# Optimization experiments

Hardware: AMD Instinct MI355X
Metric: run time of the kernel (lower is better)

Reference implementation:

```python
import jax, jax.numpy as jnp
import numpy as np

K = 3  # TAGConv default number of hops
N, E = 50000, 800000
F_X, F_POS, HID, OUT = 6, 2, 64, 10


def _tagconv(x, W, b, src, dst, norm, n):
    # TAGConv: out = sum_{k=0}^{K} (A_norm^k x) @ W[k] + b
    out = x @ W[0]
    h = x
    for k in range(1, K + 1):
        # one propagate step: gather from src, weight, scatter-sum to dst
        h = jax.ops.segment_sum(norm[:, None] * h[src], dst, num_segments=n)
        out = out + h @ W[k]
    return out + b


def setup_inputs() -> dict:
    key = jax.random.key(0)
    ks = jax.random.split(key, 12)
    x = jax.random.normal(ks[0], (N, F_X), dtype=jnp.float32)
    pos = jax.random.normal(ks[1], (N, F_POS), dtype=jnp.float32)
    edge_index = jax.random.randint(ks[2], (2, E), 0, N, dtype=jnp.int64)
    edge_attr = jax.random.uniform(ks[3], (E,), dtype=jnp.float32)
    s = 0.1
    W1 = jax.random.normal(ks[4], (K + 1, F_X + F_POS, HID), dtype=jnp.float32) * s
    b1 = jnp.zeros((HID,), dtype=jnp.float32)
    W2 = jax.random.normal(ks[5], (K + 1, HID, HID), dtype=jnp.float32) * s
    b2 = jnp.zeros((HID,), dtype=jnp.float32)
    W3 = jax.random.normal(ks[6], (K + 1, HID, OUT), dtype=jnp.float32) * s
    b3 = jnp.zeros((OUT,), dtype=jnp.float32)
    return {"x": x, "pos": pos, "edge_attr": edge_attr,
            "W1": W1, "b1": b1, "W2": W2, "b2": b2, "W3": W3, "b3": b3,
            "edge_index": edge_index}


def reference(x, pos, edge_attr, W1, b1, W2, b2, W3, b3, edge_index):
    n = x.shape[0]
    src, dst = edge_index[0], edge_index[1]
    # gcn_norm (no self loops, as in TAGConv): deg over destination (col)
    deg = jax.ops.segment_sum(edge_attr, dst, num_segments=n)
    dinv = jnp.where(deg > 0, jax.lax.rsqrt(deg), jnp.zeros_like(deg))
    norm = dinv[src] * edge_attr * dinv[dst]
    h = jnp.concatenate([x, pos], axis=1)
    h = jax.nn.relu(_tagconv(h, W1, b1, src, dst, norm, n))
    # F.dropout with training=False is identity (eval reference)
    h = jax.nn.relu(_tagconv(h, W2, b2, src, dst, norm, n))
    h = _tagconv(h, W3, b3, src, dst, norm, n)
    return jax.nn.log_softmax(h, axis=1)
```

## Files before the change

kernel.cpp:

```cpp
#include <hip/hip_runtime.h>
#include <math.h>


#define NN 50000
#define EE 800000
#define HID 64
#define NOUT 10
#define CH 512

#define NB 391
#define CAP 2400
#define K1_EPB 4096

__device__ __forceinline__ unsigned bf16rnd(float x) {
    unsigned u = __float_as_uint(x);
    return (u + 0x7FFFu + ((u >> 16) & 1u)) >> 16;
}
__device__ __forceinline__ unsigned packbf2(float a, float b) {
    return bf16rnd(a) | (bf16rnd(b) << 16);
}
__device__ __forceinline__ float bflo(unsigned u) { return __uint_as_float(u << 16); }
__device__ __forceinline__ float bfhi(unsigned u) { return __uint_as_float(u & 0xFFFF0000u); }

__global__ __launch_bounds__(512) void bucket_scatter_kernel(
        const int* __restrict__ src, const int* __restrict__ dst,
        const float* __restrict__ ea, int* __restrict__ cursor,
        int2* __restrict__ regions, int e) {
    __shared__ int hist[NB];
    __shared__ int base[NB];
    int tid = threadIdx.x;
    int e0 = blockIdx.x * K1_EPB;
    int e1 = e0 + K1_EPB; if (e1 > e) e1 = e;
    for (int i = tid; i < NB; i += 512) hist[i] = 0;
    __syncthreads();
    for (int i = e0 + tid; i < e1; i += 512)
        atomicAdd(&hist[dst[i] >> 7], 1);
    __syncthreads();
    for (int b = tid; b < NB; b += 512) {
        int c = hist[b];
        base[b] = (c > 0) ? atomicAdd(&cursor[b], c) : 0;
        hist[b] = 0;
    }
    __syncthreads();
    for (int i = e0 + tid; i < e1; i += 512) {
        int d = dst[i];
        int b = d >> 7;
        int r = atomicAdd(&hist[b], 1);
        int pos = base[b] + r;
        if (pos < CAP)
            regions[(size_t)b * CAP + pos] =
                make_int2(((d & 127) << 16) | src[i], __float_as_int(ea[i]));
    }
}

__global__ __launch_bounds__(512) void bucket_build_kernel(
        const int* __restrict__ cursor, int2* __restrict__ regions,
        float* __restrict__ dinv, int* __restrict__ row_start, int n) {
    __shared__ int2 rec[CAP];
    __shared__ int hist[128];
    __shared__ float easum[128];
    __shared__ float dl[128];
    __shared__ int off[129];
    __shared__ int lcur[128];
    int b = blockIdx.x;
    int tid = threadIdx.x;
    int cnt = cursor[b]; if (cnt > CAP) cnt = CAP;
    size_t rb = (size_t)b * CAP;
    if (tid < 128) { hist[tid] = 0; easum[tid] = 0.f; lcur[tid] = 0; }
    __syncthreads();
    for (int i = tid; i < cnt; i += 512) {
        int2 r = regions[rb + i];
        rec[i] = r;
        int f = r.x >> 16;
        atomicAdd(&hist[f], 1);
        atomicAdd(&easum[f], __int_as_float(r.y));
    }
    __syncthreads();
    if (tid < 128) {
        int lane = tid & 63;
        int v = hist[tid];
        for (int o2 = 1; o2 < 64; o2 <<= 1) {
            int y = __shfl_up(v, o2, 64);
            if (lane >= o2) v += y;
        }
        off[tid + 1] = v;
        float s2 = easum[tid];
        dl[tid] = (s2 > 0.f) ? rsqrtf(s2) : 0.f;
    }
    __syncthreads();
    if (tid == 255) off[0] = 0;
    if (tid >= 64 && tid < 128) off[tid + 1] += off[64];
    __syncthreads();
    if (tid < 128) {
        int node = b * 128 + tid;
        if (node <= n) row_start[node] = b * CAP + off[tid];
        if (node < n)  dinv[node] = dl[tid];
    }
    __syncthreads();
    for (int i = tid; i < cnt; i += 512) {
        int2 r = rec[i];
        int f = r.x >> 16;
        int s = r.x & 0xFFFF;
        int p = atomicAdd(&lcur[f], 1);
        float w0 = __int_as_float(r.y) * dl[f];
        regions[rb + off[f] + p] = make_int2(s, __float_as_int(w0));
    }
}

__global__ __launch_bounds__(256) void srcscale_kernel(
        const int* __restrict__ cursor, const float* __restrict__ dinv,
        int2* __restrict__ regions) {
    int i = blockIdx.x * blockDim.x + threadIdx.x;
    int b = i / CAP;
    if (b >= NB) return;
    int off = i - b * CAP;
    int cnt = cursor[b]; if (cnt > CAP) cnt = CAP;
    if (off >= cnt) return;
    int2 r = regions[i];
    r.y = __float_as_int(__int_as_float(r.y) * dinv[r.x]);
    regions[i] = r;
}

__global__ __launch_bounds__(256) void pack1_kernel(const float* __restrict__ x,
                                                    const float* __restrict__ pos,
                                                    unsigned short* __restrict__ B1, int n) {
    int i = blockIdx.x * blockDim.x + threadIdx.x;
    if (i >= n) return;
    float2 a = *reinterpret_cast<const float2*>(x + (size_t)i * 6);
    float2 b = *reinterpret_cast<const float2*>(x + (size_t)i * 6 + 2);
    float2 c = *reinterpret_cast<const float2*>(x + (size_t)i * 6 + 4);
    float2 p = *reinterpret_cast<const float2*>(pos + (size_t)i * 2);
    uint4 o;
    o.x = packbf2(a.x, a.y);
    o.y = packbf2(b.x, b.y);
    o.z = packbf2(c.x, c.y);
    o.w = packbf2(p.x, p.y);
    *reinterpret_cast<uint4*>(B1 + (size_t)i * 32) = o;
}

__global__ __launch_bounds__(256) void prop8b_kernel(const int* __restrict__ row_start,
                                                     const int* __restrict__ cursor,
                                                     const int2* __restrict__ edges,
                                                     const unsigned short* __restrict__ Gin,
                                                     unsigned short* __restrict__ Gout, int n) {
    constexpr int TEAM = 8, NPB = 32;
    __shared__ int2 se[CH];
    int tid = threadIdx.x;
    int nb = blockIdx.x * NPB;
    int node = nb + tid / TEAM;
    int es = tid % TEAM;
    int nbEnd = (nb + NPB < n) ? (nb + NPB) : n;
    int bkt = nb >> 7;
    int cc = cursor[bkt]; if (cc > CAP) cc = CAP;
    int ce = bkt * CAP + cc;
    int blkBeg = row_start[nb];
    int blkEnd = row_start[nbEnd]; if (blkEnd > ce) blkEnd = ce;
    int beg = 0, end = 0;
    if (node < n) {
        beg = row_start[node];
        end = row_start[node + 1]; if (end > ce) end = ce;
    }
    float a0 = 0.f, a1 = 0.f, a2 = 0.f, a3 = 0.f, a4 = 0.f, a5 = 0.f, a6 = 0.f, a7 = 0.f;
    for (int base = blkBeg; base < blkEnd; base += CH) {
        int m = blkEnd - base; if (m > CH) m = CH;
        __syncthreads();
        for (int i = tid; i < m; i += 256) se[i] = edges[base + i];
        __syncthreads();
        int lo = (beg > base) ? (beg - base) : 0;
        int hi = ((end < base + m) ? end : (base + m)) - base;
        for (int i = lo + es; i < hi; i += TEAM) {
            int2 e = se[i];
            float w = __int_as_float(e.y);
            const uint4 v = *reinterpret_cast<const uint4*>(Gin + (size_t)e.x * 32);
            a0 += w * bflo(v.x); a1 += w * bfhi(v.x);
            a2 += w * bflo(v.y); a3 += w * bfhi(v.y);
            a4 += w * bflo(v.z); a5 += w * bfhi(v.z);
            a6 += w * bflo(v.w); a7 += w * bfhi(v.w);
        }
    }
    #pragma unroll
    for (int msk = 1; msk < TEAM; msk <<= 1) {
        a0 += __shfl_xor(a0, msk); a1 += __shfl_xor(a1, msk);
        a2 += __shfl_xor(a2, msk); a3 += __shfl_xor(a3, msk);
        a4 += __shfl_xor(a4, msk); a5 += __shfl_xor(a5, msk);
        a6 += __shfl_xor(a6, msk); a7 += __shfl_xor(a7, msk);
    }
    if (node < n && es == 0) {
        uint4 o;
        o.x = packbf2(a0, a1);
        o.y = packbf2(a2, a3);
        o.z = packbf2(a4, a5);
        o.w = packbf2(a6, a7);
        *reinterpret_cast<uint4*>(Gout + (size_t)node * 32) = o;
    }
}

template <int TPN, int ES, bool ACC>
__global__ __launch_bounds__(256) void prop_kernel(const int* __restrict__ row_start,
                                                   const int* __restrict__ cursor,
                                                   const int2* __restrict__ edges,
                                                   const float* __restrict__ hin, int in_stride,
                                                   float* __restrict__ hout, int out_stride, int n) {
    constexpr int TEAM = TPN * ES;
    constexpr int NPB = 256 / TEAM;
    __shared__ int2 se[CH];
    int tid = threadIdx.x;
    int nb = blockIdx.x * NPB;
    int node = nb + tid / TEAM;
    int t = tid % TEAM;
    int es = t / TPN;
    int lane = t % TPN;
    int nbEnd = (nb + NPB < n) ? (nb + NPB) : n;
    int bkt = nb >> 7;
    int cc = cursor[bkt]; if (cc > CAP) cc = CAP;
    int ce = bkt * CAP + cc;
    int blkBeg = row_start[nb];
    int blkEnd = row_start[nbEnd]; if (blkEnd > ce) blkEnd = ce;
    int beg = 0, end = 0;
    if (node < n) {
        beg = row_start[node];
        end = row_start[node + 1]; if (end > ce) end = ce;
    }
    float ax = 0.f, ay = 0.f, az = 0.f, aw = 0.f;
    for (int base = blkBeg; base < blkEnd; base += CH) {
        int m = blkEnd - base; if (m > CH) m = CH;
        __syncthreads();
        for (int i = tid; i < m; i += 256) se[i] = edges[base + i];
        __syncthreads();
        int lo = (beg > base) ? (beg - base) : 0;
        int hi = ((end < base + m) ? end : (base + m)) - base;
        for (int i = lo + es; i < hi; i += ES) {
            int2 e = se[i];
            float w = __int_as_float(e.y);
            const float4 v = *reinterpret_cast<const float4*>(hin + (size_t)e.x * in_stride + lane * 4);
            ax += w * v.x; ay += w * v.y; az += w * v.z; aw += w * v.w;
        }
    }
    #pragma unroll
    for (int msk = TPN; msk < TEAM; msk <<= 1) {
        ax += __shfl_xor(ax, msk);
        ay += __shfl_xor(ay, msk);
        az += __shfl_xor(az, msk);
        aw += __shfl_xor(aw, msk);
    }
    if (node < n && es == 0) {
        float4* po = reinterpret_cast<float4*>(hout + (size_t)node * out_stride + lane * 4);
        float4 r = make_float4(ax, ay, az, aw);
        if (ACC) { float4 o = *po; r.x += o.x; r.y += o.y; r.z += o.z; r.w += o.w; }
        *po = r;
    }
}

__global__ __launch_bounds__(256) void prop64b_kernel(const int* __restrict__ row_start,
                                                      const int* __restrict__ cursor,
                                                      const int2* __restrict__ edges,
                                                      const unsigned short* __restrict__ Gin,
                                                      unsigned short* __restrict__ Gout, int n) {
    constexpr int TPN = 8, ES = 4, TEAM = 32, NPB = 8;
    __shared__ int2 se[CH];
    int tid = threadIdx.x;
    int nb = blockIdx.x * NPB;
    int node = nb + tid / TEAM;
    int t = tid % TEAM;
    int es = t / TPN;
    int lane = t % TPN;
    int nbEnd = (nb + NPB < n) ? (nb + NPB) : n;
    int bkt = nb >> 7;
    int cc = cursor[bkt]; if (cc > CAP) cc = CAP;
    int ce = bkt * CAP + cc;
    int blkBeg = row_start[nb];
    int blkEnd = row_start[nbEnd]; if (blkEnd > ce) blkEnd = ce;
    int beg = 0, end = 0;
    if (node < n) {
        beg = row_start[node];
        end = row_start[node + 1]; if (end > ce) end = ce;
    }
    float a0 = 0.f, a1 = 0.f, a2 = 0.f, a3 = 0.f, a4 = 0.f, a5 = 0.f, a6 = 0.f, a7 = 0.f;
    for (int base = blkBeg; base < blkEnd; base += CH) {
        int m = blkEnd - base; if (m > CH) m = CH;
        __syncthreads();
        for (int i = tid; i < m; i += 256) se[i] = edges[base + i];
        __syncthreads();
        int lo = (beg > base) ? (beg - base) : 0;
        int hi = ((end < base + m) ? end : (base + m)) - base;
        for (int i = lo + es; i < hi; i += ES) {
            int2 e = se[i];
            float w = __int_as_float(e.y);
            const uint4 v = *reinterpret_cast<const uint4*>(Gin + (size_t)e.x * 256 + lane * 8);
            a0 += w * bflo(v.x); a1 += w * bfhi(v.x);
            a2 += w * bflo(v.y); a3 += w * bfhi(v.y);
            a4 += w * bflo(v.z); a5 += w * bfhi(v.z);
            a6 += w * bflo(v.w); a7 += w * bfhi(v.w);
        }
    }
    #pragma unroll
    for (int msk = TPN; msk < TEAM; msk <<= 1) {
        a0 += __shfl_xor(a0, msk); a1 += __shfl_xor(a1, msk);
        a2 += __shfl_xor(a2, msk); a3 += __shfl_xor(a3, msk);
        a4 += __shfl_xor(a4, msk); a5 += __shfl_xor(a5, msk);
        a6 += __shfl_xor(a6, msk); a7 += __shfl_xor(a7, msk);
    }
    if (node < n && es == 0) {
        uint4 o;
        o.x = packbf2(a0, a1);
        o.y = packbf2(a2, a3);
        o.z = packbf2(a4, a5);
        o.w = packbf2(a6, a7);
        *reinterpret_cast<uint4*>(Gout + (size_t)node * 256 + lane * 8) = o;
    }
}

__global__ __launch_bounds__(256) void prop_final_kernel(const int* __restrict__ row_start,
                                                         const int* __restrict__ cursor,
                                                         const int2* __restrict__ edges,
                                                         const float* __restrict__ hin,
                                                         const float* __restrict__ g0,
                                                         const float* __restrict__ b3,
                                                         float* __restrict__ out, int n) {
    constexpr int TPN = 4, ES = 2, TEAM = 8, NPB = 32;
    __shared__ int2 se[CH];
    int tid = threadIdx.x;
    int nb = blockIdx.x * NPB;
    int node = nb + tid / TEAM;
    int t = tid % TEAM;
    int es = t / TPN;
    int lane = t % TPN;
    int nbEnd = (nb + NPB < n) ? (nb + NPB) : n;
    int bkt = nb >> 7;
    int cc = cursor[bkt]; if (cc > CAP) cc = CAP;
    int ce = bkt * CAP + cc;
    int blkBeg = row_start[nb];
    int blkEnd = row_start[nbEnd]; if (blkEnd > ce) blkEnd = ce;
    int beg = 0, end = 0;
    if (node < n) {
        beg = row_start[node];
        end = row_start[node + 1]; if (end > ce) end = ce;
    }
    float ax = 0.f, ay = 0.f, az = 0.f, aw = 0.f;
    for (int base = blkBeg; base < blkEnd; base += CH) {
        int m = blkEnd - base; if (m > CH) m = CH;
        __syncthreads();
        for (int i = tid; i < m; i += 256) se[i] = edges[base + i];
        __syncthreads();
        int lo = (beg > base) ? (beg - base) : 0;
        int hi = ((end < base + m) ? end : (base + m)) - base;
        for (int i = lo + es; i < hi; i += ES) {
            int2 e = se[i];
            float w = __int_as_float(e.y);
            const float4 v = *reinterpret_cast<const float4*>(hin + (size_t)e.x * 64 + lane * 4);
            ax += w * v.x; ay += w * v.y; az += w * v.z; aw += w * v.w;
        }
    }
    ax += __shfl_xor(ax, TPN);
    ay += __shfl_xor(ay, TPN);
    az += __shfl_xor(az, TPN);
    aw += __shfl_xor(aw, TPN);
    if (node < n && es == 0) {
        const float4 g = *reinterpret_cast<const float4*>(g0 + (size_t)node * 64 + lane * 4);
        float vv[4] = {ax + g.x, ay + g.y, az + g.z, aw + g.w};
        int c0 = lane * 4;
        float mloc = -1e30f;
        #pragma unroll
        for (int c = 0; c < 4; ++c) {
            int col = c0 + c;
            if (col < NOUT) { vv[c] += b3[col]; mloc = fmaxf(mloc, vv[c]); }
        }
        float mo = fmaxf(mloc, __shfl_xor(mloc, 1));
        mo = fmaxf(mo, __shfl_xor(mo, 2));
        float sl = 0.f;
        #pragma unroll
        for (int c = 0; c < 4; ++c) {
            int col = c0 + c;
            if (col < NOUT) sl += __expf(vv[c] - mo);
        }
        sl += __shfl_xor(sl, 1);
        sl += __shfl_xor(sl, 2);
        float ls = __logf(sl);
        #pragma unroll
        for (int c = 0; c < 4; ++c) {
            int col = c0 + c;
            if (col < NOUT) out[(size_t)node * NOUT + col] = vv[c] - mo - ls;
        }
    }
}

template <int FIN, int KC, int EPI, int WMODE, int INBF16, int OUTBF16>
__global__ __launch_bounds__(256) void mm2_kernel(const void* __restrict__ hraw, int hstride,
                                                  const float* __restrict__ W,
                                                  const float* __restrict__ bias,
                                                  void* __restrict__ outraw, int ostride, int n) {
    constexpr int HP = 68;
    __shared__ float HsT[KC * HP];
    __shared__ float Ws[KC * 64];
    int tid = threadIdx.x;
    int ndq = tid >> 4;
    int f4  = tid & 15;
    int nd  = tid & 63;
    int wv  = tid >> 6;
    int nodeBase = blockIdx.x * 64;

    float4 acc0 = make_float4(0.f, 0.f, 0.f, 0.f);
    float4 acc1 = make_float4(0.f, 0.f, 0.f, 0.f);
    float4 acc2 = make_float4(0.f, 0.f, 0.f, 0.f);
    float4 acc3 = make_float4(0.f, 0.f, 0.f, 0.f);

    for (int kc = 0; kc < FIN; kc += KC) {
        if (WMODE == 0) {
            for (int i = tid * 4; i < KC * 64; i += 1024)
                *reinterpret_cast<float4*>(&Ws[i]) =
                    *reinterpret_cast<const float4*>(&W[(size_t)kc * 64 + i]);
        } else {
            for (int i = tid; i < KC * 64; i += 256) {
                int r = i >> 6, c = i & 63;
                int k = c >> 4, j = c & 15;
                Ws[i] = (j < NOUT) ? W[((size_t)k * FIN + kc + r) * NOUT + j] : 0.f;
            }
        }
        int node = nodeBase + nd;
        if constexpr (INBF16) {
            const unsigned short* hb = (const unsigned short*)hraw;
            constexpr int KPT = KC / 4;
            int k0 = wv * KPT;
            #pragma unroll
            for (int q = 0; q < KPT / 8; ++q) {
                uint4 v = make_uint4(0, 0, 0, 0);
                if (node < n)
                    v = *reinterpret_cast<const uint4*>(hb + (size_t)node * hstride + kc + k0 + q * 8);
                int kk = k0 + q * 8;
                HsT[(kk + 0) * HP + nd] = bflo(v.x); HsT[(kk + 1) * HP + nd] = bfhi(v.x);
                HsT[(kk + 2) * HP + nd] = bflo(v.y); HsT[(kk + 3) * HP + nd] = bfhi(v.y);
                HsT[(kk + 4) * HP + nd] = bflo(v.z); HsT[(kk + 5) * HP + nd] = bfhi(v.z);
                HsT[(kk + 6) * HP + nd] = bflo(v.w); HsT[(kk + 7) * HP + nd] = bfhi(v.w);
            }
        } else {
            const float* hf = (const float*)hraw;
            #pragma unroll
            for (int r = 0; r < KC / 16; ++r) {
                int k0 = wv * 4 + r * 16;
                float4 hv = make_float4(0.f, 0.f, 0.f, 0.f);
                if (node < n)
                    hv = *reinterpret_cast<const float4*>(&hf[(size_t)node * hstride + kc + k0]);
                HsT[(k0 + 0) * HP + nd] = hv.x;
                HsT[(k0 + 1) * HP + nd] = hv.y;
                HsT[(k0 + 2) * HP + nd] = hv.z;
                HsT[(k0 + 3) * HP + nd] = hv.w;
            }
        }
        __syncthreads();
        #pragma unroll 8
        for (int k = 0; k < KC; ++k) {
            const float4 hq = *reinterpret_cast<const float4*>(&HsT[k * HP + ndq * 4]);
            const float4 wq = *reinterpret_cast<const float4*>(&Ws[k * 64 + f4 * 4]);
            acc0.x += hq.x * wq.x; acc0.y += hq.x * wq.y; acc0.z += hq.x * wq.z; acc0.w += hq.x * wq.w;
            acc1.x += hq.y * wq.x; acc1.y += hq.y * wq.y; acc1.z += hq.y * wq.z; acc1.w += hq.y * wq.w;
            acc2.x += hq.z * wq.x; acc2.y += hq.z * wq.y; acc2.z += hq.z * wq.z; acc2.w += hq.z * wq.w;
            acc3.x += hq.w * wq.x; acc3.y += hq.w * wq.y; acc3.z += hq.w * wq.z; acc3.w += hq.w * wq.w;
        }
        __syncthreads();
    }

    float4 bv = make_float4(0.f, 0.f, 0.f, 0.f);
    if (EPI == 1) bv = *reinterpret_cast<const float4*>(&bias[f4 * 4]);
    float4 accs[4] = {acc0, acc1, acc2, acc3};
    #pragma unroll
    for (int i = 0; i < 4; ++i) {
        int node = nodeBase + ndq * 4 + i;
        if (node < n) {
            float4 a = accs[i];
            if (EPI == 1) {
                a.x = fmaxf(a.x + bv.x, 0.f); a.y = fmaxf(a.y + bv.y, 0.f);
                a.z = fmaxf(a.z + bv.z, 0.f); a.w = fmaxf(a.w + bv.w, 0.f);
            }
            if constexpr (OUTBF16) {
                unsigned short* ob = (unsigned short*)outraw;
                uint2 o;
                o.x = packbf2(a.x, a.y);
                o.y = packbf2(a.z, a.w);
                *reinterpret_cast<uint2*>(ob + (size_t)node * ostride + f4 * 4) = o;
            } else {
                float* of = (float*)outraw;
                *reinterpret_cast<float4*>(of + (size_t)node * ostride + f4 * 4) = a;
            }
        }
    }
}

__global__ __launch_bounds__(256) void mm23_kernel(const unsigned short* __restrict__ G,
                                                   const float* __restrict__ W2,
                                                   const float* __restrict__ b2,
                                                   const float* __restrict__ W3,
                                                   float* __restrict__ T, int n) {
    constexpr int HP = 68;
    __shared__ float HsT[64 * HP];
    __shared__ float Ws[64 * 64];
    int tid = threadIdx.x;
    int ndq = tid >> 4;
    int f4  = tid & 15;
    int nd  = tid & 63;
    int wv  = tid >> 6;
    int nodeBase = blockIdx.x * 64;

    float4 acc0 = make_float4(0.f, 0.f, 0.f, 0.f);
    float4 acc1 = make_float4(0.f, 0.f, 0.f, 0.f);
    float4 acc2 = make_float4(0.f, 0.f, 0.f, 0.f);
    float4 acc3 = make_float4(0.f, 0.f, 0.f, 0.f);

    for (int kc = 0; kc < 256; kc += 64) {
        for (int i = tid * 4; i < 64 * 64; i += 1024)
            *reinterpret_cast<float4*>(&Ws[i]) =
                *reinterpret_cast<const float4*>(&W2[(size_t)kc * 64 + i]);
        int node = nodeBase + nd;
        int k0 = wv * 16;
        uint4 q0 = make_uint4(0, 0, 0, 0), q1 = make_uint4(0, 0, 0, 0);
        if (node < n) {
            const unsigned short* row = G + (size_t)node * 256 + kc + k0;
            q0 = *reinterpret_cast<const uint4*>(row);
            q1 = *reinterpret_cast<const uint4*>(row + 8);
        }
        HsT[(k0 + 0) * HP + nd] = bflo(q0.x);  HsT[(k0 + 1) * HP + nd] = bfhi(q0.x);
        HsT[(k0 + 2) * HP + nd] = bflo(q0.y);  HsT[(k0 + 3) * HP + nd] = bfhi(q0.y);
        HsT[(k0 + 4) * HP + nd] = bflo(q0.z);  HsT[(k0 + 5) * HP + nd] = bfhi(q0.z);
        HsT[(k0 + 6) * HP + nd] = bflo(q0.w);  HsT[(k0 + 7) * HP + nd] = bfhi(q0.w);
        HsT[(k0 + 8) * HP + nd] = bflo(q1.x);  HsT[(k0 + 9) * HP + nd] = bfhi(q1.x);
        HsT[(k0 + 10) * HP + nd] = bflo(q1.y); HsT[(k0 + 11) * HP + nd] = bfhi(q1.y);
        HsT[(k0 + 12) * HP + nd] = bflo(q1.z); HsT[(k0 + 13) * HP + nd] = bfhi(q1.z);
        HsT[(k0 + 14) * HP + nd] = bflo(q1.w); HsT[(k0 + 15) * HP + nd] = bfhi(q1.w);
        __syncthreads();
        #pragma unroll 8
        for (int k = 0; k < 64; ++k) {
            const float4 hq = *reinterpret_cast<const float4*>(&HsT[k * HP + ndq * 4]);
            const float4 wq = *reinterpret_cast<const float4*>(&Ws[k * 64 + f4 * 4]);
            acc0.x += hq.x * wq.x; acc0.y += hq.x * wq.y; acc0.z += hq.x * wq.z; acc0.w += hq.x * wq.w;
            acc1.x += hq.y * wq.x; acc1.y += hq.y * wq.y; acc1.z += hq.y * wq.z; acc1.w += hq.y * wq.w;
            acc2.x += hq.z * wq.x; acc2.y += hq.z * wq.y; acc2.z += hq.z * wq.z; acc2.w += hq.z * wq.w;
            acc3.x += hq.w * wq.x; acc3.y += hq.w * wq.y; acc3.z += hq.w * wq.z; acc3.w += hq.w * wq.w;
        }
        __syncthreads();
    }

    {
        const float4 bv = *reinterpret_cast<const float4*>(&b2[f4 * 4]);
        float4 accs[4] = {acc0, acc1, acc2, acc3};
        #pragma unroll
        for (int i = 0; i < 4; ++i) {
            float4 a = accs[i];
            a.x = fmaxf(a.x + bv.x, 0.f); a.y = fmaxf(a.y + bv.y, 0.f);
            a.z = fmaxf(a.z + bv.z, 0.f); a.w = fmaxf(a.w + bv.w, 0.f);
            int col = ndq * 4 + i;
            HsT[(f4 * 4 + 0) * HP + col] = a.x;
            HsT[(f4 * 4 + 1) * HP + col] = a.y;
            HsT[(f4 * 4 + 2) * HP + col] = a.z;
            HsT[(f4 * 4 + 3) * HP + col] = a.w;
        }
    }
    __syncthreads();
    for (int i = tid; i < 64 * 64; i += 256) {
        int r = i >> 6, c = i & 63;
        int k = c >> 4, j = c & 15;
        Ws[i] = (j < NOUT) ? W3[((size_t)k * 64 + r) * NOUT + j] : 0.f;
    }
    __syncthreads();
    float4 t0 = make_float4(0.f, 0.f, 0.f, 0.f);
    float4 t1 = make_float4(0.f, 0.f, 0.f, 0.f);
    float4 t2 = make_float4(0.f, 0.f, 0.f, 0.f);
    float4 t3 = make_float4(0.f, 0.f, 0.f, 0.f);
    #pragma unroll 8
    for (int k = 0; k < 64; ++k) {
        const float4 hq = *reinterpret_cast<const float4*>(&HsT[k * HP + ndq * 4]);
        const float4 wq = *reinterpret_cast<const float4*>(&Ws[k * 64 + f4 * 4]);
        t0.x += hq.x * wq.x; t0.y += hq.x * wq.y; t0.z += hq.x * wq.z; t0.w += hq.x * wq.w;
        t1.x += hq.y * wq.x; t1.y += hq.y * wq.y; t1.z += hq.y * wq.z; t1.w += hq.y * wq.w;
        t2.x += hq.z * wq.x; t2.y += hq.z * wq.y; t2.z += hq.z * wq.z; t2.w += hq.z * wq.w;
        t3.x += hq.w * wq.x; t3.y += hq.w * wq.y; t3.z += hq.w * wq.z; t3.w += hq.w * wq.w;
    }
    float4 ts[4] = {t0, t1, t2, t3};
    #pragma unroll
    for (int i = 0; i < 4; ++i) {
        int node = nodeBase + ndq * 4 + i;
        if (node < n)
            *reinterpret_cast<float4*>(T + (size_t)node * 64 + f4 * 4) = ts[i];
    }
}

extern "C" void kernel_launch(void* const* d_in, const int* in_sizes, int n_in,
                              void* d_out, int out_size, void* d_ws, size_t ws_size,
                              hipStream_t stream) {
    const float* x   = (const float*)d_in[0];
    const float* pos = (const float*)d_in[1];
    const float* ea  = (const float*)d_in[2];
    const float* W1  = (const float*)d_in[3];
    const float* b1  = (const float*)d_in[4];
    const float* W2  = (const float*)d_in[5];
    const float* b2  = (const float*)d_in[6];
    const float* W3  = (const float*)d_in[7];
    const float* b3  = (const float*)d_in[8];
    const int* eidx  = (const int*)d_in[9];
    const int* src = eidx;
    const int* dst = eidx + EE;
    float* outp = (float*)d_out;

    size_t off = 0;
    char* base = (char*)d_ws;
    auto alloc = [&](size_t bytes) -> void* {
        void* p = base + off;
        off += (bytes + 255) & ~(size_t)255;
        return p;
    };
    int*   cursor    = (int*)alloc(NB * 4);
    int*   row_start = (int*)alloc((NN + 1) * 4);
    float* dinv      = (float*)alloc(NN * 4);
    int2*  edges     = (int2*)alloc((size_t)NB * CAP * 8);
    unsigned short* G  = (unsigned short*)alloc((size_t)NN * 256 * 2);
    unsigned short* B1 = (unsigned short*)alloc((size_t)NN * 32 * 2);
    float* T         = (float*)alloc((size_t)NN * 64 * 4);
    (void)ws_size;

    const int B = 256;
    const int gN = (NN + B - 1) / B;
    const int gK1 = (EE + K1_EPB - 1) / K1_EPB;
    const int gK3 = (NB * CAP + B - 1) / B;
    const int gMM2 = (NN + 63) / 64;
    const int gP32 = (NN + 31) / 32;
    const int gP8  = (NN + 7) / 8;

    hipMemsetAsync(cursor, 0, NB * 4, stream);

    bucket_scatter_kernel<<<gK1, 512, 0, stream>>>(src, dst, ea, cursor, edges, EE);
    bucket_build_kernel<<<NB, 512, 0, stream>>>(cursor, edges, dinv, row_start, NN);
    srcscale_kernel<<<gK3, B, 0, stream>>>(cursor, dinv, edges);

    pack1_kernel<<<gN, B, 0, stream>>>(x, pos, B1, NN);
    prop8b_kernel<<<gP32, B, 0, stream>>>(row_start, cursor, edges, B1,      B1 + 8,  NN);
    prop8b_kernel<<<gP32, B, 0, stream>>>(row_start, cursor, edges, B1 + 8,  B1 + 16, NN);
    prop8b_kernel<<<gP32, B, 0, stream>>>(row_start, cursor, edges, B1 + 16, B1 + 24, NN);
    mm2_kernel<32, 32, 1, 0, 1, 1><<<gMM2, B, 0, stream>>>(B1, 32, W1, b1, G, 256, NN);

    prop64b_kernel<<<gP8, B, 0, stream>>>(row_start, cursor, edges, G,       G + 64,  NN);
    prop64b_kernel<<<gP8, B, 0, stream>>>(row_start, cursor, edges, G + 64,  G + 128, NN);
    prop64b_kernel<<<gP8, B, 0, stream>>>(row_start, cursor, edges, G + 128, G + 192, NN);
    mm23_kernel<<<gMM2, B, 0, stream>>>(G, W2, b2, W3, T, NN);

    prop_kernel<4, 2, true><<<gP32, B, 0, stream>>>(row_start, cursor, edges, T + 48, 64, T + 32, 64, NN);
    prop_kernel<4, 2, true><<<gP32, B, 0, stream>>>(row_start, cursor, edges, T + 32, 64, T + 16, 64, NN);
    prop_final_kernel<<<gP32, B, 0, stream>>>(row_start, cursor, edges, T + 16, T, b3, outp, NN);
}
```

Before: 300.3 us.

## Use bf16 MFMA for layer-2 dense GEMM in mm23 kernel

Replaces the scalar FP32 outer-product loop over the 256x64 layer-2 weight with 16x16x32 bf16 MFMA instructions. Each block converts W2 to bf16 in a swizzled shared-memory layout, and each wave loads its A fragments straight from the bf16 G rows, removing the transpose staging through shared memory. This cuts ALU and shared-memory traffic for the GEMM, but every block now re-converts W2 to bf16, and the weights lose precision compared with the FP32 path.

New measurement: 279.4 us. -6.9%, faster.

```diff
diff --git a/kernel.cpp b/kernel.cpp
--- a/kernel.cpp
+++ b/kernel.cpp
@@ -11,6 +11,9 @@
 #define NB 391
 #define CAP 2400
 #define K1_EPB 4096
+
+typedef __attribute__((ext_vector_type(8))) short bf16x8;
+typedef __attribute__((ext_vector_type(4))) float f32x4;
 
 __device__ __forceinline__ unsigned bf16rnd(float x) {
     unsigned u = __float_as_uint(x);
@@ -491,75 +494,74 @@
                                                    const float* __restrict__ W3,
                                                    float* __restrict__ T, int n) {
     constexpr int HP = 68;
-    __shared__ float HsT[64 * HP];
-    __shared__ float Ws[64 * 64];
-    int tid = threadIdx.x;
+    __shared__ __align__(16) char smem[33792];
+    unsigned short* w2s = (unsigned short*)smem;
+    float* HsT = (float*)smem;
+    float* Ws  = (float*)(smem + 64 * HP * 4);
+    int tid = threadIdx.x;
+    int wave = tid >> 6;
+    int lane = tid & 63;
+    int nodeBase = blockIdx.x * 64;
+
+    for (int slot = tid; slot < 2048; slot += 256) {
+        int l = slot & 63;
+        int s = (slot >> 6) & 7;
+        int t = slot >> 9;
+        int k0 = s * 32 + ((l >> 4) << 3);
+        int col = t * 16 + (l & 15);
+        unsigned short tmp[8];
+        #pragma unroll
+        for (int j = 0; j < 8; ++j)
+            tmp[j] = (unsigned short)bf16rnd(W2[(size_t)(k0 + j) * 64 + col]);
+        *reinterpret_cast<uint4*>(w2s + slot * 8) = *reinterpret_cast<const uint4*>(tmp);
+    }
+    __syncthreads();
+
+    int arow = nodeBase + wave * 16 + (lane & 15);
+    bool aval = (arow < n);
+    const unsigned short* arp = G + (size_t)arow * 256 + ((lane >> 4) << 3);
+    f32x4 acc0 = {0.f, 0.f, 0.f, 0.f}, acc1 = {0.f, 0.f, 0.f, 0.f};
+    f32x4 acc2 = {0.f, 0.f, 0.f, 0.f}, acc3 = {0.f, 0.f, 0.f, 0.f};
+    #pragma unroll
+    for (int s = 0; s < 8; ++s) {
+        bf16x8 a = {};
+        if (aval) a = *reinterpret_cast<const bf16x8*>(arp + s * 32);
+        const unsigned short* wb = w2s + ((size_t)s * 64 + lane) * 8;
+        bf16x8 bf0 = *reinterpret_cast<const bf16x8*>(wb);
+        bf16x8 bf1 = *reinterpret_cast<const bf16x8*>(wb + 4096);
+        bf16x8 bf2 = *reinterpret_cast<const bf16x8*>(wb + 8192);
+        bf16x8 bf3 = *reinterpret_cast<const bf16x8*>(wb + 12288);
+        acc0 = __builtin_amdgcn_mfma_f32_16x16x32_bf16(a, bf0, acc0, 0, 0, 0);
+        acc1 = __builtin_amdgcn_mfma_f32_16x16x32_bf16(a, bf1, acc1, 0, 0, 0);
+        acc2 = __builtin_amdgcn_mfma_f32_16x16x32_bf16(a, bf2, acc2, 0, 0, 0);
+        acc3 = __builtin_amdgcn_mfma_f32_16x16x32_bf16(a, bf3, acc3, 0, 0, 0);
+    }
+    __syncthreads();
+
+    {
+        int c = lane & 15;
+        int rbase = wave * 16 + (lane >> 4) * 4;
+        f32x4 accs[4] = {acc0, acc1, acc2, acc3};
+        #pragma unroll
+        for (int t = 0; t < 4; ++t) {
+            int col = t * 16 + c;
+            float bb = b2[col];
+            #pragma unroll
+            for (int r = 0; r < 4; ++r) {
+                float v = accs[t][r] + bb;
+                HsT[col * HP + rbase + r] = v > 0.f ? v : 0.f;
+            }
+        }
+    }
+    for (int i = tid; i < 64 * 64; i += 256) {
+        int r = i >> 6, c2 = i & 63;
+        int k = c2 >> 4, j = c2 & 15;
+        Ws[i] = (j < NOUT) ? W3[((size_t)k * 64 + r) * NOUT + j] : 0.f;
+    }
+    __syncthreads();
+
     int ndq = tid >> 4;
     int f4  = tid & 15;
-    int nd  = tid & 63;
-    int wv  = tid >> 6;
-    int nodeBase = blockIdx.x * 64;
-
-    float4 acc0 = make_float4(0.f, 0.f, 0.f, 0.f);
-    float4 acc1 = make_float4(0.f, 0.f, 0.f, 0.f);
-    float4 acc2 = make_float4(0.f, 0.f, 0.f, 0.f);
-    float4 acc3 = make_float4(0.f, 0.f, 0.f, 0.f);
-
-    for (int kc = 0; kc < 256; kc += 64) {
-        for (int i = tid * 4; i < 64 * 64; i += 1024)
-            *reinterpret_cast<float4*>(&Ws[i]) =
-                *reinterpret_cast<const float4*>(&W2[(size_t)kc * 64 + i]);
-        int node = nodeBase + nd;
-        int k0 = wv * 16;
-        uint4 q0 = make_uint4(0, 0, 0, 0), q1 = make_uint4(0, 0, 0, 0);
-        if (node < n) {
-            const unsigned short* row = G + (size_t)node * 256 + kc + k0;
-            q0 = *reinterpret_cast<const uint4*>(row);
-            q1 = *reinterpret_cast<const uint4*>(row + 8);
-        }
-        HsT[(k0 + 0) * HP + nd] = bflo(q0.x);  HsT[(k0 + 1) * HP + nd] = bfhi(q0.x);
-        HsT[(k0 + 2) * HP + nd] = bflo(q0.y);  HsT[(k0 + 3) * HP + nd] = bfhi(q0.y);
-        HsT[(k0 + 4) * HP + nd] = bflo(q0.z);  HsT[(k0 + 5) * HP + nd] = bfhi(q0.z);
-        HsT[(k0 + 6) * HP + nd] = bflo(q0.w);  HsT[(k0 + 7) * HP + nd] = bfhi(q0.w);
-        HsT[(k0 + 8) * HP + nd] = bflo(q1.x);  HsT[(k0 + 9) * HP + nd] = bfhi(q1.x);
-        HsT[(k0 + 10) * HP + nd] = bflo(q1.y); HsT[(k0 + 11) * HP + nd] = bfhi(q1.y);
-        HsT[(k0 + 12) * HP + nd] = bflo(q1.z); HsT[(k0 + 13) * HP + nd] = bfhi(q1.z);
-        HsT[(k0 + 14) * HP + nd] = bflo(q1.w); HsT[(k0 + 15) * HP + nd] = bfhi(q1.w);
-        __syncthreads();
-        #pragma unroll 8
-        for (int k = 0; k < 64; ++k) {
-            const float4 hq = *reinterpret_cast<const float4*>(&HsT[k * HP + ndq * 4]);
-            const float4 wq = *reinterpret_cast<const float4*>(&Ws[k * 64 + f4 * 4]);
-            acc0.x += hq.x * wq.x; acc0.y += hq.x * wq.y; acc0.z += hq.x * wq.z; acc0.w += hq.x * wq.w;
-            acc1.x += hq.y * wq.x; acc1.y += hq.y * wq.y; acc1.z += hq.y * wq.z; acc1.w += hq.y * wq.w;
-            acc2.x += hq.z * wq.x; acc2.y += hq.z * wq.y; acc2.z += hq.z * wq.z; acc2.w += hq.z * wq.w;
-            acc3.x += hq.w * wq.x; acc3.y += hq.w * wq.y; acc3.z += hq.w * wq.z; acc3.w += hq.w * wq.w;
-        }
-        __syncthreads();
-    }
-
-    {
-        const float4 bv = *reinterpret_cast<const float4*>(&b2[f4 * 4]);
-        float4 accs[4] = {acc0, acc1, acc2, acc3};
-        #pragma unroll
-        for (int i = 0; i < 4; ++i) {
-            float4 a = accs[i];
-            a.x = fmaxf(a.x + bv.x, 0.f); a.y = fmaxf(a.y + bv.y, 0.f);
-            a.z = fmaxf(a.z + bv.z, 0.f); a.w = fmaxf(a.w + bv.w, 0.f);
-            int col = ndq * 4 + i;
-            HsT[(f4 * 4 + 0) * HP + col] = a.x;
-            HsT[(f4 * 4 + 1) * HP + col] = a.y;
-            HsT[(f4 * 4 + 2) * HP + col] = a.z;
-            HsT[(f4 * 4 + 3) * HP + col] = a.w;
-        }
-    }
-    __syncthreads();
-    for (int i = tid; i < 64 * 64; i += 256) {
-        int r = i >> 6, c = i & 63;
-        int k = c >> 4, j = c & 15;
-        Ws[i] = (j < NOUT) ? W3[((size_t)k * 64 + r) * NOUT + j] : 0.f;
-    }
-    __syncthreads();
     float4 t0 = make_float4(0.f, 0.f, 0.f, 0.f);
     float4 t1 = make_float4(0.f, 0.f, 0.f, 0.f);
     float4 t2 = make_float4(0.f, 0.f, 0.f, 0.f);
```
